# Kernel optimization log

Hardware: AMD Instinct MI355X
Metric: run time of the kernel (lower is better)

The kernel has to match this reference:

```python
import jax, jax.numpy as jnp
import numpy as np

EPS = 1e-8  # torch cosine_similarity eps


def setup_inputs() -> dict:
    key = jax.random.key(0)
    k1, k2, k3 = jax.random.split(key, 3)
    N, D, n_classes = 512, 512, 10
    prediction = jax.random.normal(k1, (N, D), dtype=jnp.float32)
    # raw (pre-softplus) learnable distances, n_classes - 1 of them
    distances_raw = jax.random.uniform(k2, (n_classes - 1,), dtype=jnp.float32)
    target = jax.random.randint(k3, (N,), 0, n_classes)
    return {"prediction": prediction, "distances_raw": distances_raw, "target": target}


def reference(prediction, distances_raw, target):
    N = prediction.shape[0]
    # cosine similarity matrix [N, N]
    norms = jnp.linalg.norm(prediction, axis=1, keepdims=True)
    xn = prediction / jnp.maximum(norms, EPS)
    cos = xn @ xn.T

    same = target[:, None] == target[None, :]
    eye = jnp.eye(N, dtype=bool)
    positives = same & ~eye          # same-class pairs, excluding self
    negatives = ~same                # different-class pairs (diag excluded since same)

    # ordinal class positions on a line; pairwise class-center distances
    pos_d = jax.nn.softplus(distances_raw)
    class_pos = jnp.concatenate([jnp.zeros((1,), cos.dtype), jnp.cumsum(pos_d)])
    dist_matrix = jnp.abs(class_pos[:, None] - class_pos[None, :])
    margins = dist_matrix[target[:, None], target[None, :]]
    margins = jnp.where(negatives, margins, 0.0)

    # term[i, j, k] = relu(cos[i,j] + margin[i,j] - cos[i,k]),
    # valid only when (i,j) is a negative pair and (i,k) is a positive pair.
    term = jax.nn.relu((cos + margins)[:, :, None] - cos[:, None, :])  # [i,j,k]
    term = term * negatives[:, :, None].astype(cos.dtype) * positives[:, None, :].astype(cos.dtype)

    S = term.sum(axis=1)                                  # [i, k]
    n_neg = negatives.sum(axis=1).astype(cos.dtype)       # [i]
    count = positives.astype(cos.dtype) * n_neg[:, None]  # [i, k] valid-pair counts
    loss_ik = S / jnp.maximum(count, 1.0)

    # aggregate over positive anchors k, then mean over samples i
    tot = (loss_ik * (count > 0)).sum(axis=1) / jnp.maximum(count.sum(axis=1), 1.0)
    return tot.mean()
```

## Files before the change

kernel.cpp:

```cpp
#include <hip/hip_runtime.h>
#include <math.h>

#define N 512
#define D 512
#define NC 10
#define EPSF 1e-8f

typedef __attribute__((ext_vector_type(8))) __bf16 bf16x8;
typedef __attribute__((ext_vector_type(4))) float f32x4;

__device__ __forceinline__ unsigned short f2bf_rne(float f) {
  unsigned u = __float_as_uint(f);
  u += 0x7fffu + ((u >> 16) & 1u);
  return (unsigned short)(u >> 16);
}
__device__ __forceinline__ float bf2f(unsigned short h) {
  return __uint_as_float(((unsigned)h) << 16);
}

__global__ __launch_bounds__(256) void k_convert(
    const float* __restrict__ pred, const float* __restrict__ dist_raw,
    unsigned short* __restrict__ XH, unsigned short* __restrict__ XL,
    float* __restrict__ class_pos, float* __restrict__ out) {
  const int idx = blockIdx.x * 256 + threadIdx.x;
  float4 v = ((const float4*)pred)[idx];
  ushort4 h, l;
  h.x = f2bf_rne(v.x); l.x = f2bf_rne(v.x - bf2f(h.x));
  h.y = f2bf_rne(v.y); l.y = f2bf_rne(v.y - bf2f(h.y));
  h.z = f2bf_rne(v.z); l.z = f2bf_rne(v.z - bf2f(h.z));
  h.w = f2bf_rne(v.w); l.w = f2bf_rne(v.w - bf2f(h.w));
  ((ushort4*)XH)[idx] = h;
  ((ushort4*)XL)[idx] = l;
  if (idx == 0) {
    out[0] = 0.0f;
    float acc = 0.0f;
    class_pos[0] = 0.0f;
    for (int c = 0; c < NC - 1; ++c) {
      acc += log1pf(expf(dist_raw[c]));
      class_pos[c + 1] = acc;
    }
  }
}

__global__ __launch_bounds__(256) void k_gram(
    const unsigned short* __restrict__ XH, const unsigned short* __restrict__ XL,
    float* __restrict__ G, float* __restrict__ inv_n) {
  __shared__ unsigned short LB[4][32][256];

  const int t = threadIdx.x;
  const int lane = t & 63;
  const int wid = t >> 6;
  const int bi = blockIdx.y, bj = blockIdx.x;

  const unsigned short* __restrict__ srcArr = (wid & 1) ? XL : XH;
  const int tileBase = ((wid < 2) ? bi : bj) * 32;

  const int frow = lane & 15;
  const int kg = lane >> 4;
  const int wr = wid >> 1, wc = wid & 1;
  const int arow = wr * 16 + frow;
  const int brow = wc * 16 + frow;

  f32x4 ahh = {0.f, 0.f, 0.f, 0.f};
  f32x4 ahl = ahh, alh = ahh, all_ = ahh;

  for (int c = 0; c < 2; ++c) {
#pragma unroll
    for (int i = 0; i < 16; ++i) {
      const int gr = i * 64 + lane;
      const int row = gr >> 5;
      const int gsw = (lane & 31) ^ (row & 7);
      const unsigned short* src =
          srcArr + (size_t)(tileBase + row) * D + c * 256 + gsw * 8;
      unsigned short* dst = &LB[wid][0][0] + (size_t)i * 64 * 8;
      __builtin_amdgcn_global_load_lds(
          (const __attribute__((address_space(1))) void*)src,
          (__attribute__((address_space(3))) void*)dst, 16, 0, 0);
    }
    __syncthreads();
#pragma unroll
    for (int kc = 0; kc < 8; ++kc) {
      const int ga = (((kc * 4 + kg) ^ (arow & 7))) * 8;
      const int gb = (((kc * 4 + kg) ^ (brow & 7))) * 8;
      bf16x8 ah = *(const bf16x8*)&LB[0][arow][ga];
      bf16x8 al = *(const bf16x8*)&LB[1][arow][ga];
      bf16x8 bh = *(const bf16x8*)&LB[2][brow][gb];
      bf16x8 bl = *(const bf16x8*)&LB[3][brow][gb];
      ahh = __builtin_amdgcn_mfma_f32_16x16x32_bf16(ah, bh, ahh, 0, 0, 0);
      ahl = __builtin_amdgcn_mfma_f32_16x16x32_bf16(ah, bl, ahl, 0, 0, 0);
      alh = __builtin_amdgcn_mfma_f32_16x16x32_bf16(al, bh, alh, 0, 0, 0);
      all_ = __builtin_amdgcn_mfma_f32_16x16x32_bf16(al, bl, all_, 0, 0, 0);
    }
    __syncthreads();
  }

  const int gcol = bj * 32 + wc * 16 + frow;
  const int grow0 = bi * 32 + wr * 16 + kg * 4;
#pragma unroll
  for (int r = 0; r < 4; ++r) {
    const float v = ahh[r] + all_[r] + (ahl[r] + alh[r]);
    G[(size_t)(grow0 + r) * N + gcol] = v;
    if (bi == bj && (grow0 + r) == gcol)
      inv_n[gcol] = 1.0f / fmaxf(sqrtf(v), EPSF);
  }
}

__global__ __launch_bounds__(256) void k_rows(
    const float* __restrict__ G, const int* __restrict__ target,
    const float* __restrict__ inv_n, const float* __restrict__ class_pos,
    float* __restrict__ out) {
  const int i = blockIdx.x;
  const int tid = threadIdx.x;

  __shared__ float s_p[N];
  __shared__ float s_cp[16];
  __shared__ int s_np;
  __shared__ float s_part[4];

  if (tid == 0) s_np = 0;
  if (tid < NC) s_cp[tid] = class_pos[tid];
  __syncthreads();

  const int ti = target[i];
  const float inv_i = inv_n[i];
  const float cpi = s_cp[ti];

  float a0, a1;
  {
    const int j = tid;
    const float cosv = G[(size_t)i * N + j] * inv_i * inv_n[j];
    const int tj = target[j];
    if (tj != ti) {
      a0 = cosv + fabsf(cpi - s_cp[tj]);
    } else {
      a0 = -1e30f;
      if (j != i) { int k = atomicAdd(&s_np, 1); s_p[k] = cosv; }
    }
  }
  {
    const int j = tid + 256;
    const float cosv = G[(size_t)i * N + j] * inv_i * inv_n[j];
    const int tj = target[j];
    if (tj != ti) {
      a1 = cosv + fabsf(cpi - s_cp[tj]);
    } else {
      a1 = -1e30f;
      if (j != i) { int k = atomicAdd(&s_np, 1); s_p[k] = cosv; }
    }
  }
  __syncthreads();

  const int np = s_np;
  const int nn = N - 1 - np;
  float acc = 0.0f;
  for (int kk = 0; kk < np; ++kk) {
    const float ck = s_p[kk];
    acc += fmaxf(a0 - ck, 0.0f) + fmaxf(a1 - ck, 0.0f);
  }

#pragma unroll
  for (int off = 32; off > 0; off >>= 1) acc += __shfl_down(acc, off);
  if ((tid & 63) == 0) s_part[tid >> 6] = acc;
  __syncthreads();
  if (tid == 0) {
    const float total = s_part[0] + s_part[1] + s_part[2] + s_part[3];
    if (np > 0 && nn > 0) {
      atomicAdd(out, total / ((float)nn * (float)nn * (float)np) / (float)N);
    }
  }
}

extern "C" void kernel_launch(void* const* d_in, const int* in_sizes, int n_in,
                              void* d_out, int out_size, void* d_ws, size_t ws_size,
                              hipStream_t stream) {
  const float* pred = (const float*)d_in[0];
  const float* dist_raw = (const float*)d_in[1];
  const int* target = (const int*)d_in[2];
  float* out = (float*)d_out;

  float* G = (float*)d_ws;
  float* inv_n = G + (size_t)N * N;
  float* class_pos = inv_n + N;
  unsigned short* XH = (unsigned short*)(class_pos + 16);
  unsigned short* XL = XH + (size_t)N * D;

  k_convert<<<256, 256, 0, stream>>>(pred, dist_raw, XH, XL, class_pos, out);
  k_gram<<<dim3(16, 16), 256, 0, stream>>>(XH, XL, G, inv_n);
  k_rows<<<N, 256, 0, stream>>>(G, target, inv_n, class_pos, out);
}
```

Before: 75.63 us.

## Fuse convert, gram and row-loss kernels into one cooperative kernel with grid syncs

Replaces the three kernel launches with a single cooperative kernel of 256 blocks that uses grid-wide syncs between the conversion, Gram MFMA, and per-row loss phases. Row norms are now computed directly from fp32 inputs during conversion instead of from the Gram diagonal, and each block processes two rows in the loss phase. This aims to remove launch gaps and inter-kernel overhead, at the cost of grid-sync latency and cooperative-launch constraints. The row phase now uses 256 blocks instead of 512, which halves parallelism there.

```diff
diff --git a/kernel.cpp b/kernel.cpp
--- a/kernel.cpp
+++ b/kernel.cpp
@@ -1,5 +1,8 @@
 #include <hip/hip_runtime.h>
+#include <hip/hip_cooperative_groups.h>
 #include <math.h>
+
+namespace cg = cooperative_groups;
 
 #define N 512
 #define D 512
@@ -18,154 +21,174 @@
   return __uint_as_float(((unsigned)h) << 16);
 }
 
-__global__ __launch_bounds__(256) void k_convert(
+__global__ __launch_bounds__(256) void k_all(
     const float* __restrict__ pred, const float* __restrict__ dist_raw,
+    const int* __restrict__ target,
     unsigned short* __restrict__ XH, unsigned short* __restrict__ XL,
+    float* __restrict__ G, float* __restrict__ inv_n,
     float* __restrict__ class_pos, float* __restrict__ out) {
-  const int idx = blockIdx.x * 256 + threadIdx.x;
-  float4 v = ((const float4*)pred)[idx];
-  ushort4 h, l;
-  h.x = f2bf_rne(v.x); l.x = f2bf_rne(v.x - bf2f(h.x));
-  h.y = f2bf_rne(v.y); l.y = f2bf_rne(v.y - bf2f(h.y));
-  h.z = f2bf_rne(v.z); l.z = f2bf_rne(v.z - bf2f(h.z));
-  h.w = f2bf_rne(v.w); l.w = f2bf_rne(v.w - bf2f(h.w));
-  ((ushort4*)XH)[idx] = h;
-  ((ushort4*)XL)[idx] = l;
-  if (idx == 0) {
-    out[0] = 0.0f;
-    float acc = 0.0f;
-    class_pos[0] = 0.0f;
-    for (int c = 0; c < NC - 1; ++c) {
-      acc += log1pf(expf(dist_raw[c]));
-      class_pos[c + 1] = acc;
-    }
-  }
-}
-
-__global__ __launch_bounds__(256) void k_gram(
-    const unsigned short* __restrict__ XH, const unsigned short* __restrict__ XL,
-    float* __restrict__ G, float* __restrict__ inv_n) {
-  __shared__ unsigned short LB[4][32][256];
-
-  const int t = threadIdx.x;
-  const int lane = t & 63;
-  const int wid = t >> 6;
-  const int bi = blockIdx.y, bj = blockIdx.x;
-
-  const unsigned short* __restrict__ srcArr = (wid & 1) ? XL : XH;
-  const int tileBase = ((wid < 2) ? bi : bj) * 32;
-
-  const int frow = lane & 15;
-  const int kg = lane >> 4;
-  const int wr = wid >> 1, wc = wid & 1;
-  const int arow = wr * 16 + frow;
-  const int brow = wc * 16 + frow;
-
-  f32x4 ahh = {0.f, 0.f, 0.f, 0.f};
-  f32x4 ahl = ahh, alh = ahh, all_ = ahh;
-
-  for (int c = 0; c < 2; ++c) {
-#pragma unroll
-    for (int i = 0; i < 16; ++i) {
-      const int gr = i * 64 + lane;
-      const int row = gr >> 5;
-      const int gsw = (lane & 31) ^ (row & 7);
-      const unsigned short* src =
-          srcArr + (size_t)(tileBase + row) * D + c * 256 + gsw * 8;
-      unsigned short* dst = &LB[wid][0][0] + (size_t)i * 64 * 8;
-      __builtin_amdgcn_global_load_lds(
-          (const __attribute__((address_space(1))) void*)src,
-          (__attribute__((address_space(3))) void*)dst, 16, 0, 0);
-    }
+  __shared__ __align__(16) unsigned char smraw[4 * 32 * 256 * 2];
+
+  const int tid = threadIdx.x;
+  const int bid = blockIdx.x;
+  const int lane = tid & 63;
+  const int wid = tid >> 6;
+  cg::grid_group grid = cg::this_grid();
+
+  {
+    const int row = bid * 2 + (tid >> 7);
+    const int c4 = tid & 127;
+    float4 v = ((const float4*)(pred + (size_t)row * D))[c4];
+    ushort4 h, l;
+    h.x = f2bf_rne(v.x); l.x = f2bf_rne(v.x - bf2f(h.x));
+    h.y = f2bf_rne(v.y); l.y = f2bf_rne(v.y - bf2f(h.y));
+    h.z = f2bf_rne(v.z); l.z = f2bf_rne(v.z - bf2f(h.z));
+    h.w = f2bf_rne(v.w); l.w = f2bf_rne(v.w - bf2f(h.w));
+    ((ushort4*)(XH + (size_t)row * D))[c4] = h;
+    ((ushort4*)(XL + (size_t)row * D))[c4] = l;
+
+    float p = v.x * v.x + v.y * v.y + v.z * v.z + v.w * v.w;
+#pragma unroll
+    for (int off = 32; off > 0; off >>= 1) p += __shfl_down(p, off);
+    float* wsum = (float*)smraw;
+    if (lane == 0) wsum[wid] = p;
     __syncthreads();
-#pragma unroll
-    for (int kc = 0; kc < 8; ++kc) {
-      const int ga = (((kc * 4 + kg) ^ (arow & 7))) * 8;
-      const int gb = (((kc * 4 + kg) ^ (brow & 7))) * 8;
-      bf16x8 ah = *(const bf16x8*)&LB[0][arow][ga];
-      bf16x8 al = *(const bf16x8*)&LB[1][arow][ga];
-      bf16x8 bh = *(const bf16x8*)&LB[2][brow][gb];
-      bf16x8 bl = *(const bf16x8*)&LB[3][brow][gb];
-      ahh = __builtin_amdgcn_mfma_f32_16x16x32_bf16(ah, bh, ahh, 0, 0, 0);
-      ahl = __builtin_amdgcn_mfma_f32_16x16x32_bf16(ah, bl, ahl, 0, 0, 0);
-      alh = __builtin_amdgcn_mfma_f32_16x16x32_bf16(al, bh, alh, 0, 0, 0);
-      all_ = __builtin_amdgcn_mfma_f32_16x16x32_bf16(al, bl, all_, 0, 0, 0);
+    if (tid == 0) {
+      inv_n[bid * 2]     = 1.0f / fmaxf(sqrtf(wsum[0] + wsum[1]), EPSF);
+      inv_n[bid * 2 + 1] = 1.0f / fmaxf(sqrtf(wsum[2] + wsum[3]), EPSF);
+    }
+    if (bid == 0 && tid == 64) {
+      out[0] = 0.0f;
+      float acc = 0.0f;
+      class_pos[0] = 0.0f;
+      for (int c = 0; c < NC - 1; ++c) {
+        acc += log1pf(expf(dist_raw[c]));
+        class_pos[c + 1] = acc;
+      }
     }
     __syncthreads();
   }
-
-  const int gcol = bj * 32 + wc * 16 + frow;
-  const int grow0 = bi * 32 + wr * 16 + kg * 4;
-#pragma unroll
-  for (int r = 0; r < 4; ++r) {
-    const float v = ahh[r] + all_[r] + (ahl[r] + alh[r]);
-    G[(size_t)(grow0 + r) * N + gcol] = v;
-    if (bi == bj && (grow0 + r) == gcol)
-      inv_n[gcol] = 1.0f / fmaxf(sqrtf(v), EPSF);
+  __threadfence();
+  grid.sync();
+
+  {
+    typedef unsigned short LBrow[32][256];
+    LBrow* LB = (LBrow*)smraw;
+    const int bi = bid >> 4, bj = bid & 15;
+
+    const unsigned short* __restrict__ srcArr = (wid & 1) ? XL : XH;
+    const int tileBase = ((wid < 2) ? bi : bj) * 32;
+
+    const int frow = lane & 15;
+    const int kg = lane >> 4;
+    const int wr = wid >> 1, wc = wid & 1;
+    const int arow = wr * 16 + frow;
+    const int brow = wc * 16 + frow;
+
+    f32x4 ahh = {0.f, 0.f, 0.f, 0.f};
+    f32x4 ahl = ahh, alh = ahh, all_ = ahh;
+
+    for (int c = 0; c < 2; ++c) {
+#pragma unroll
+      for (int i = 0; i < 16; ++i) {
+        const int gr = i * 64 + lane;
+        const int row = gr >> 5;
+        const int gsw = (lane & 31) ^ (row & 7);
+        const unsigned short* src =
+            srcArr + (size_t)(tileBase + row) * D + c * 256 + gsw * 8;
+        unsigned short* dst = &LB[wid][0][0] + (size_t)i * 64 * 8;
+        __builtin_amdgcn_global_load_lds(
+            (const __attribute__((address_space(1))) void*)src,
+            (__attribute__((address_space(3))) void*)dst, 16, 0, 0);
+      }
+      __syncthreads();
+#pragma unroll
+      for (int kc = 0; kc < 8; ++kc) {
+        const int ga = ((kc * 4 + kg) ^ (arow & 7)) * 8;
+        const int gb = ((kc * 4 + kg) ^ (brow & 7)) * 8;
+        bf16x8 ah = *(const bf16x8*)&LB[0][arow][ga];
+        bf16x8 al = *(const bf16x8*)&LB[1][arow][ga];
+        bf16x8 bh = *(const bf16x8*)&LB[2][brow][gb];
+        bf16x8 bl = *(const bf16x8*)&LB[3][brow][gb];
+        ahh = __builtin_amdgcn_mfma_f32_16x16x32_bf16(ah, bh, ahh, 0, 0, 0);
+        ahl = __builtin_amdgcn_mfma_f32_16x16x32_bf16(ah, bl, ahl, 0, 0, 0);
+        alh = __builtin_amdgcn_mfma_f32_16x16x32_bf16(al, bh, alh, 0, 0, 0);
+        all_ = __builtin_amdgcn_mfma_f32_16x16x32_bf16(al, bl, all_, 0, 0, 0);
+      }
+      __syncthreads();
+    }
+
+    const int gcol = bj * 32 + wc * 16 + frow;
+    const int grow0 = bi * 32 + wr * 16 + kg * 4;
+#pragma unroll
+    for (int r = 0; r < 4; ++r) {
+      G[(size_t)(grow0 + r) * N + gcol] = ahh[r] + all_[r] + (ahl[r] + alh[r]);
+    }
   }
-}
-
-__global__ __launch_bounds__(256) void k_rows(
-    const float* __restrict__ G, const int* __restrict__ target,
-    const float* __restrict__ inv_n, const float* __restrict__ class_pos,
-    float* __restrict__ out) {
-  const int i = blockIdx.x;
-  const int tid = threadIdx.x;
-
-  __shared__ float s_p[N];
-  __shared__ float s_cp[16];
-  __shared__ int s_np;
-  __shared__ float s_part[4];
-
-  if (tid == 0) s_np = 0;
-  if (tid < NC) s_cp[tid] = class_pos[tid];
-  __syncthreads();
-
-  const int ti = target[i];
-  const float inv_i = inv_n[i];
-  const float cpi = s_cp[ti];
-
-  float a0, a1;
+  __threadfence();
+  grid.sync();
+
   {
-    const int j = tid;
-    const float cosv = G[(size_t)i * N + j] * inv_i * inv_n[j];
-    const int tj = target[j];
-    if (tj != ti) {
-      a0 = cosv + fabsf(cpi - s_cp[tj]);
-    } else {
-      a0 = -1e30f;
-      if (j != i) { int k = atomicAdd(&s_np, 1); s_p[k] = cosv; }
-    }
-  }
-  {
-    const int j = tid + 256;
-    const float cosv = G[(size_t)i * N + j] * inv_i * inv_n[j];
-    const int tj = target[j];
-    if (tj != ti) {
-      a1 = cosv + fabsf(cpi - s_cp[tj]);
-    } else {
-      a1 = -1e30f;
-      if (j != i) { int k = atomicAdd(&s_np, 1); s_p[k] = cosv; }
-    }
-  }
-  __syncthreads();
-
-  const int np = s_np;
-  const int nn = N - 1 - np;
-  float acc = 0.0f;
-  for (int kk = 0; kk < np; ++kk) {
-    const float ck = s_p[kk];
-    acc += fmaxf(a0 - ck, 0.0f) + fmaxf(a1 - ck, 0.0f);
-  }
-
-#pragma unroll
-  for (int off = 32; off > 0; off >>= 1) acc += __shfl_down(acc, off);
-  if ((tid & 63) == 0) s_part[tid >> 6] = acc;
-  __syncthreads();
-  if (tid == 0) {
-    const float total = s_part[0] + s_part[1] + s_part[2] + s_part[3];
-    if (np > 0 && nn > 0) {
-      atomicAdd(out, total / ((float)nn * (float)nn * (float)np) / (float)N);
+    float* s_p = (float*)smraw;
+    float* s_cp = (float*)(smraw + 2176);
+    int* s_np = (int*)(smraw + 2304);
+    float* s_part = (float*)(smraw + 2368);
+
+    if (tid < NC) s_cp[tid] = class_pos[tid];
+
+    for (int rr = 0; rr < 2; ++rr) {
+      const int i = bid * 2 + rr;
+      if (tid == 0) *s_np = 0;
+      __syncthreads();
+
+      const int ti = target[i];
+      const float inv_i = inv_n[i];
+      const float cpi = s_cp[ti];
+
+      float a0, a1;
+      {
+        const int j = tid;
+        const float cosv = G[(size_t)i * N + j] * inv_i * inv_n[j];
+        const int tj = target[j];
+        if (tj != ti) {
+          a0 = cosv + fabsf(cpi - s_cp[tj]);
+        } else {
+          a0 = -1e30f;
+          if (j != i) { int k = atomicAdd(s_np, 1); s_p[k] = cosv; }
+        }
+      }
+      {
+        const int j = tid + 256;
+        const float cosv = G[(size_t)i * N + j] * inv_i * inv_n[j];
+        const int tj = target[j];
+        if (tj != ti) {
+          a1 = cosv + fabsf(cpi - s_cp[tj]);
+        } else {
+          a1 = -1e30f;
+          if (j != i) { int k = atomicAdd(s_np, 1); s_p[k] = cosv; }
+        }
+      }
+      __syncthreads();
+
+      const int np = *s_np;
+      const int nn = N - 1 - np;
+      float acc = 0.0f;
+      for (int kk = 0; kk < np; ++kk) {
+        const float ck = s_p[kk];
+        acc += fmaxf(a0 - ck, 0.0f) + fmaxf(a1 - ck, 0.0f);
+      }
+
+#pragma unroll
+      for (int off = 32; off > 0; off >>= 1) acc += __shfl_down(acc, off);
+      if (lane == 0) s_part[wid] = acc;
+      __syncthreads();
+      if (tid == 0) {
+        const float total = s_part[0] + s_part[1] + s_part[2] + s_part[3];
+        if (np > 0 && nn > 0) {
+          atomicAdd(out, total / ((float)nn * (float)nn * (float)np) / (float)N);
+        }
+      }
+      __syncthreads();
     }
   }
 }
@@ -184,7 +207,9 @@
   unsigned short* XH = (unsigned short*)(class_pos + 16);
   unsigned short* XL = XH + (size_t)N * D;
 
-  k_convert<<<256, 256, 0, stream>>>(pred, dist_raw, XH, XL, class_pos, out);
-  k_gram<<<dim3(16, 16), 256, 0, stream>>>(XH, XL, G, inv_n);
-  k_rows<<<N, 256, 0, stream>>>(G, target, inv_n, class_pos, out);
-}
+  void* args[] = {(void*)&pred, (void*)&dist_raw, (void*)&target,
+                  (void*)&XH,   (void*)&XL,       (void*)&G,
+                  (void*)&inv_n, (void*)&class_pos, (void*)&out};
+  hipLaunchCooperativeKernel((const void*)k_all, dim3(256), dim3(256), args, 0,
+                             stream);
+}
```

Result: slower. 169.6 us (+124.3%).

## Fuse bf16 hi/lo split into Gram kernel with register-prefetched fp32 loads

Applied to the files above, without the earlier changes.

Removes the separate conversion kernel and instead loads fp32 rows of the input directly in the Gram kernel, splitting them into bf16 high/low parts in registers before writing to LDS. The second K-half is prefetched into registers while the MFMAs on the first half run. This drops one kernel launch and the round trip of the bf16 copies through global memory. In exchange the conversion work is repeated by every tile block (16x redundancy per row) and the kernel uses more registers. Class positions and output zeroing move into block (0,0) of the Gram kernel.

```diff
diff --git a/kernel.cpp b/kernel.cpp
--- a/kernel.cpp
+++ b/kernel.cpp
@@ -9,29 +9,18 @@
 typedef __attribute__((ext_vector_type(8))) __bf16 bf16x8;
 typedef __attribute__((ext_vector_type(4))) float f32x4;
 
-__device__ __forceinline__ unsigned short f2bf_rne(float f) {
-  unsigned u = __float_as_uint(f);
-  u += 0x7fffu + ((u >> 16) & 1u);
-  return (unsigned short)(u >> 16);
-}
-__device__ __forceinline__ float bf2f(unsigned short h) {
-  return __uint_as_float(((unsigned)h) << 16);
-}
+__global__ __launch_bounds__(256) void k_gram(
+    const float* __restrict__ pred, const float* __restrict__ dist_raw,
+    float* __restrict__ G, float* __restrict__ inv_n,
+    float* __restrict__ class_pos, float* __restrict__ out) {
+  __shared__ unsigned short LB[4][32][256];
 
-__global__ __launch_bounds__(256) void k_convert(
-    const float* __restrict__ pred, const float* __restrict__ dist_raw,
-    unsigned short* __restrict__ XH, unsigned short* __restrict__ XL,
-    float* __restrict__ class_pos, float* __restrict__ out) {
-  const int idx = blockIdx.x * 256 + threadIdx.x;
-  float4 v = ((const float4*)pred)[idx];
-  ushort4 h, l;
-  h.x = f2bf_rne(v.x); l.x = f2bf_rne(v.x - bf2f(h.x));
-  h.y = f2bf_rne(v.y); l.y = f2bf_rne(v.y - bf2f(h.y));
-  h.z = f2bf_rne(v.z); l.z = f2bf_rne(v.z - bf2f(h.z));
-  h.w = f2bf_rne(v.w); l.w = f2bf_rne(v.w - bf2f(h.w));
-  ((ushort4*)XH)[idx] = h;
-  ((ushort4*)XL)[idx] = l;
-  if (idx == 0) {
+  const int t = threadIdx.x;
+  const int lane = t & 63;
+  const int wid = t >> 6;
+  const int bi = blockIdx.y, bj = blockIdx.x;
+
+  if (bi == 0 && bj == 0 && t == 0) {
     out[0] = 0.0f;
     float acc = 0.0f;
     class_pos[0] = 0.0f;
@@ -40,20 +29,10 @@
       class_pos[c + 1] = acc;
     }
   }
-}
 
-__global__ __launch_bounds__(256) void k_gram(
-    const unsigned short* __restrict__ XH, const unsigned short* __restrict__ XL,
-    float* __restrict__ G, float* __restrict__ inv_n) {
-  __shared__ unsigned short LB[4][32][256];
-
-  const int t = threadIdx.x;
-  const int lane = t & 63;
-  const int wid = t >> 6;
-  const int bi = blockIdx.y, bj = blockIdx.x;
-
-  const unsigned short* __restrict__ srcArr = (wid & 1) ? XL : XH;
-  const int tileBase = ((wid < 2) ? bi : bj) * 32;
+  const int p = wid >> 1;
+  const int sub = wid & 1;
+  const int tileBase = (p ? bj : bi) * 32;
 
   const int frow = lane & 15;
   const int kg = lane >> 4;
@@ -64,24 +43,54 @@
   f32x4 ahh = {0.f, 0.f, 0.f, 0.f};
   f32x4 ahl = ahh, alh = ahh, all_ = ahh;
 
+  float4 st[16];
+
+#pragma unroll
+  for (int it = 0; it < 8; ++it) {
+    const int gr = sub * 512 + it * 64 + lane;
+    const int row = gr >> 5, gpos = gr & 31;
+    const int glog = gpos ^ (row & 7);
+    const float* s = pred + (size_t)(tileBase + row) * D + glog * 8;
+    st[2 * it] = *(const float4*)(s);
+    st[2 * it + 1] = *(const float4*)(s + 4);
+  }
+
   for (int c = 0; c < 2; ++c) {
 #pragma unroll
-    for (int i = 0; i < 16; ++i) {
-      const int gr = i * 64 + lane;
-      const int row = gr >> 5;
-      const int gsw = (lane & 31) ^ (row & 7);
-      const unsigned short* src =
-          srcArr + (size_t)(tileBase + row) * D + c * 256 + gsw * 8;
-      unsigned short* dst = &LB[wid][0][0] + (size_t)i * 64 * 8;
-      __builtin_amdgcn_global_load_lds(
-          (const __attribute__((address_space(1))) void*)src,
-          (__attribute__((address_space(3))) void*)dst, 16, 0, 0);
+    for (int it = 0; it < 8; ++it) {
+      const int gr = sub * 512 + it * 64 + lane;
+      const int row = gr >> 5, gpos = gr & 31;
+      const float f[8] = {st[2 * it].x,     st[2 * it].y,     st[2 * it].z,
+                          st[2 * it].w,     st[2 * it + 1].x, st[2 * it + 1].y,
+                          st[2 * it + 1].z, st[2 * it + 1].w};
+      bf16x8 hv, lv;
+#pragma unroll
+      for (int k = 0; k < 8; ++k) {
+        const __bf16 h = (__bf16)f[k];
+        hv[k] = h;
+        lv[k] = (__bf16)(f[k] - (float)h);
+      }
+      *(bf16x8*)&LB[2 * p][row][gpos * 8] = hv;
+      *(bf16x8*)&LB[2 * p + 1][row][gpos * 8] = lv;
     }
     __syncthreads();
+
+    if (c == 0) {
+#pragma unroll
+      for (int it = 0; it < 8; ++it) {
+        const int gr = sub * 512 + it * 64 + lane;
+        const int row = gr >> 5, gpos = gr & 31;
+        const int glog = gpos ^ (row & 7);
+        const float* s = pred + (size_t)(tileBase + row) * D + 256 + glog * 8;
+        st[2 * it] = *(const float4*)(s);
+        st[2 * it + 1] = *(const float4*)(s + 4);
+      }
+    }
+
 #pragma unroll
     for (int kc = 0; kc < 8; ++kc) {
-      const int ga = (((kc * 4 + kg) ^ (arow & 7))) * 8;
-      const int gb = (((kc * 4 + kg) ^ (brow & 7))) * 8;
+      const int ga = ((kc * 4 + kg) ^ (arow & 7)) * 8;
+      const int gb = ((kc * 4 + kg) ^ (brow & 7)) * 8;
       bf16x8 ah = *(const bf16x8*)&LB[0][arow][ga];
       bf16x8 al = *(const bf16x8*)&LB[1][arow][ga];
       bf16x8 bh = *(const bf16x8*)&LB[2][brow][gb];
@@ -181,10 +190,8 @@
   float* G = (float*)d_ws;
   float* inv_n = G + (size_t)N * N;
   float* class_pos = inv_n + N;
-  unsigned short* XH = (unsigned short*)(class_pos + 16);
-  unsigned short* XL = XH + (size_t)N * D;
 
-  k_convert<<<256, 256, 0, stream>>>(pred, dist_raw, XH, XL, class_pos, out);
-  k_gram<<<dim3(16, 16), 256, 0, stream>>>(XH, XL, G, inv_n);
+  k_gram<<<dim3(16, 16), 256, 0, stream>>>(pred, dist_raw, G, inv_n, class_pos,
+                                           out);
   k_rows<<<N, 256, 0, stream>>>(G, target, inv_n, class_pos, out);
 }
```

After: 72.59 us. 1.04x faster.
